# Kernel optimization log

Measured on AMD Instinct MI355X. Metric: run time of the kernel, lower is better.

## Reference

```python
import jax, jax.numpy as jnp
import numpy as np

B, S, D = 16, 512, 2048
NUM_HEADS, NUM_GROUPS = 16, 4
HEAD_DIM = D // NUM_HEADS  # 128
MAX_SEQ_LEN, SHARED_SLOTS = 512, 32
EPS = 1e-6


def _rope_tables(seq_positions):
    # inv_freq over half the head dim, as in the module
    inv_freq = 1.0 / (10000.0 ** (jnp.arange(0, HEAD_DIM, 2, dtype=jnp.float32) / HEAD_DIM))
    freqs = jnp.outer(seq_positions.astype(jnp.float32), inv_freq)  # [S, HEAD_DIM//2]
    return jnp.cos(freqs), jnp.sin(freqs)


def _apply_rope(x, cos, sin):
    # x: [b, s, h, head_dim]; cos/sin: [s, 1, head_dim//2] (broadcast over heads)
    x1, x2 = jnp.split(x, 2, axis=-1)
    real = x1 * cos - x2 * sin
    imag = x1 * sin + x2 * cos
    return jnp.concatenate([real, imag], axis=-1).astype(x.dtype)


def _rmsnorm(x, scale):
    # flax RMSNorm with dtype=float32: compute in fp32
    x = x.astype(jnp.float32)
    ms = jnp.mean(jnp.square(x), axis=-1, keepdims=True)
    return x * jax.lax.rsqrt(ms + EPS) * scale


def setup_inputs() -> dict:
    key = jax.random.key(0)
    ks = jax.random.split(key, 10)
    w = 0.02
    return {
        "x": jax.random.normal(ks[0], (B, S, D), dtype=jnp.float32),
        "wq": jax.random.normal(ks[1], (D, D), dtype=jnp.float32) * w,
        "bq": jnp.zeros((D,), dtype=jnp.float32),
        "wk": jax.random.normal(ks[2], (D, NUM_GROUPS * HEAD_DIM), dtype=jnp.float32) * w,
        "bk": jnp.zeros((NUM_GROUPS * HEAD_DIM,), dtype=jnp.float32),
        "wv": jax.random.normal(ks[3], (D, NUM_GROUPS * HEAD_DIM), dtype=jnp.float32) * w,
        "bv": jnp.zeros((NUM_GROUPS * HEAD_DIM,), dtype=jnp.float32),
        "wo": jax.random.normal(ks[4], (D, D), dtype=jnp.float32) * w,
        "bo": jnp.zeros((D,), dtype=jnp.float32),
        "q_norm_scale": jnp.ones((HEAD_DIM,), dtype=jnp.float32),
        "k_norm_scale": jnp.ones((HEAD_DIM,), dtype=jnp.float32),
    }


def reference(x, wq, bq, wk, bk, wv, bv, wo, bo, q_norm_scale, k_norm_scale):
    b, s, d = x.shape
    rep = NUM_HEADS // NUM_GROUPS
    head_scale = HEAD_DIM ** (-0.5)  # applied once explicitly by the module

    # nnx.Linear(dtype=float16): projections computed in fp16
    xh = x.astype(jnp.float16)
    q = (xh @ wq.astype(jnp.float16) + bq.astype(jnp.float16)).reshape(b, s, NUM_HEADS, HEAD_DIM)
    k = (xh @ wk.astype(jnp.float16) + bk.astype(jnp.float16)).reshape(b, s, NUM_GROUPS, HEAD_DIM)
    v = (xh @ wv.astype(jnp.float16) + bv.astype(jnp.float16)).reshape(b, s, NUM_GROUPS, HEAD_DIM)

    # QK RMSNorm (fp32)
    q = _rmsnorm(q, q_norm_scale)
    k = _rmsnorm(k, k_norm_scale)

    # RoPE (default positions 0..s-1)
    pos = jnp.arange(s)
    cos, sin = _rope_tables(pos)
    cos = cos[:, None, :]
    sin = sin[:, None, :]
    q = _apply_rope(q, cos, sin) * head_scale
    k = _apply_rope(k, cos, sin)

    q = q.astype(jnp.float16)
    k = k.astype(jnp.float16)
    v = v.astype(jnp.float16)

    # GQA without materializing repeated k/v: [b, s, groups, rep, head_dim]
    qg = q.reshape(b, s, NUM_GROUPS, rep, HEAD_DIM)
    # dot_product_attention applies its own 1/sqrt(head_dim) (double-scale, faithful)
    logits = jnp.einsum('btgrh,bsgh->bgrts', qg, k,
                        preferred_element_type=jnp.float32) * head_scale

    causal = pos[:, None] >= pos[None, :]  # [s, s]
    logits = jnp.where(causal[None, None, None, :, :], logits, jnp.finfo(jnp.float32).min)
    probs = jax.nn.softmax(logits, axis=-1).astype(jnp.float16)

    out = jnp.einsum('bgrts,bsgh->btgrh', probs, v)  # [b, s, groups, rep, head_dim]
    out = out.reshape(b, s, d)
    return out @ wo.astype(jnp.float16) + bo.astype(jnp.float16)
```

## Files before the change

kernel.cpp:

```cpp
#include <hip/hip_runtime.h>

#define NB 16
#define NS 512
#define ND 2048
#define NH 16
#define NG 4
#define NHD 128
#define NM (NB * NS)
#define NKD (NG * NHD)
#define NKV 1024
#define HEAD_SCALE 0.08838834764831845f

typedef _Float16 h8 __attribute__((ext_vector_type(8)));
typedef float fx4 __attribute__((ext_vector_type(4)));

__device__ __forceinline__ void gload16(const void* g, void* l) {
  __builtin_amdgcn_global_load_lds(
      (__attribute__((address_space(1))) void*)(unsigned long long)g,
      (__attribute__((address_space(3))) void*)(unsigned long long)l,
      16, 0, 0);
}


__global__ void prep_kernel(const float* __restrict__ x, _Float16* __restrict__ xh,
                            const float* __restrict__ wq, _Float16* __restrict__ wqt,
                            const float* __restrict__ wk, const float* __restrict__ wv,
                            _Float16* __restrict__ wkvt,
                            const float* __restrict__ wo, _Float16* __restrict__ wot,
                            float* __restrict__ cosT, float* __restrict__ sinT,
                            const float* __restrict__ bk, const float* __restrict__ bv,
                            float* __restrict__ bkv) {
  __shared__ float t[64][65];
  const int bid = blockIdx.x, tid = threadIdx.x;
  if (bid < 2048) {
    const fx4* p = (const fx4*)x;
    h8* o = (h8*)xh;
#pragma unroll
    for (int it = 0; it < 4; ++it) {
      int i = (it * 2048 + bid) * 256 + tid;
      fx4 a = p[2 * i], b = p[2 * i + 1];
      h8 hv;
      hv[0] = (_Float16)a[0]; hv[1] = (_Float16)a[1]; hv[2] = (_Float16)a[2]; hv[3] = (_Float16)a[3];
      hv[4] = (_Float16)b[0]; hv[5] = (_Float16)b[1]; hv[6] = (_Float16)b[2]; hv[7] = (_Float16)b[3];
      o[i] = hv;
    }
    return;
  }
  int lb = bid - 2048;
  const float* src;
  _Float16* dst;
  int K, N;
  if (lb < 1024)      { src = wq; dst = wqt; K = ND; N = ND; }
  else if (lb < 1280) { lb -= 1024; src = wk; dst = wkvt; K = ND; N = NKD; }
  else if (lb < 1536) { lb -= 1280; src = wv; dst = wkvt + (size_t)NKD * ND; K = ND; N = NKD; }
  else if (lb < 2560) { lb -= 1536; src = wo; dst = wot; K = ND; N = ND; }
  else if (lb < 2688) {
    int i = (lb - 2560) * 256 + tid;
    int s = i >> 6, f = i & 63;
    float inv = exp2f(-(float)f * (13.287712379549449f / 64.0f));
    float a = (float)s * inv;
    cosT[i] = cosf(a);
    sinT[i] = sinf(a);
    return;
  } else {
#pragma unroll
    for (int it = 0; it < 4; ++it) {
      int idx = it * 256 + tid;
      bkv[idx] = (idx < NKD) ? bk[idx] : bv[idx - NKD];
    }
    return;
  }
  const int ntil = N >> 6;
  const int n0 = (lb % ntil) * 64, k0 = (lb / ntil) * 64;
#pragma unroll
  for (int it = 0; it < 16; ++it) {
    int idx = it * 256 + tid;
    int r = idx >> 6, c = idx & 63;
    t[r][c] = src[(size_t)(k0 + r) * N + n0 + c];
  }
  __syncthreads();
#pragma unroll
  for (int it = 0; it < 16; ++it) {
    int idx = it * 256 + tid;
    int r = idx >> 6, c = idx & 63;
    dst[(size_t)(n0 + r) * K + k0 + c] = (_Float16)t[c][r];
  }
}


__global__ void kv_post_kernel(_Float16* __restrict__ kv, _Float16* __restrict__ vt,
                               const float* __restrict__ kns,
                               const float* __restrict__ cosT, const float* __restrict__ sinT) {
  __shared__ _Float16 t[64][72];
  const int bid = blockIdx.x, tid = threadIdx.x;
  if (bid < 8192) {
    int wid = tid >> 6, lane = tid & 63;
    int task = bid * 4 + wid;
    int row = task >> 2;
    int head = task & 3;
    _Float16* p = kv + (size_t)row * NKV + head * NHD;
    float x1 = (float)p[lane], x2 = (float)p[lane + 64];
    float ss = x1 * x1 + x2 * x2;
#pragma unroll
    for (int m = 1; m < 64; m <<= 1) ss += __shfl_xor(ss, m, 64);
    float rn = rsqrtf(ss * (1.0f / 128.0f) + 1e-6f);
    int s = row & (NS - 1);
    float c = cosT[s * 64 + lane], sn = sinT[s * 64 + lane];
    float n1 = x1 * rn * kns[lane], n2 = x2 * rn * kns[64 + lane];
    p[lane] = (_Float16)(n1 * c - n2 * sn);
    p[lane + 64] = (_Float16)(n1 * sn + n2 * c);
    return;
  }
  const int v = bid - 8192;
  const int st = v & 7, dt = (v >> 3) & 1, bg = v >> 4;
  const int b = bg >> 2, g = bg & 3;
  const _Float16* src = kv + ((size_t)(b * NS + st * 64)) * NKV + NKD + g * NHD + dt * 64;
#pragma unroll
  for (int it = 0; it < 2; ++it) {
    int idx = it * 256 + tid;
    int r = idx >> 3, c = (idx & 7) * 8;
    *(h8*)&t[r][c] = *(const h8*)(src + (size_t)r * NKV + c);
  }
  __syncthreads();
  _Float16* dst = vt + ((size_t)bg * NHD + dt * 64) * NS + st * 64;
#pragma unroll
  for (int it = 0; it < 2; ++it) {
    int idx = it * 256 + tid;
    int r = idx >> 3, c = (idx & 7) * 8;
    h8 o;
#pragma unroll
    for (int e = 0; e < 8; ++e) o[e] = t[c + e][r];
    *(h8*)(dst + (size_t)r * NS + c) = o;
  }
}

__device__ __forceinline__ void st_out(float* p, float v) { *p = v; }
__device__ __forceinline__ void st_out(_Float16* p, float v) { *p = (_Float16)v; }


template <typename OT>
__global__ __launch_bounds__(256, 3) void gemm_bt_kernel(
    const _Float16* __restrict__ A, const _Float16* __restrict__ Bt,
    const float* __restrict__ bias, OT* __restrict__ C, int N, int K) {
  __shared__ alignas(16) _Float16 As[128 * 64];
  __shared__ alignas(16) _Float16 Bs[128 * 64];
  const int tid = threadIdx.x;
  const int lane = tid & 63, wid = tid >> 6;
  const int wr = wid >> 1, wc = wid & 1;
  const int la = lane & 15, lb = (lane >> 4) * 8;
  const int bm = blockIdx.y * 128, bn = blockIdx.x * 128;

  fx4 acc[4][4] = {};

  for (int kt = 0; kt < K; kt += 64) {
    const _Float16* Ag = A + (size_t)bm * K + kt;
    const _Float16* Bg = Bt + (size_t)bn * K + kt;
#pragma unroll
    for (int it = 0; it < 4; ++it) {
      int cb = it * 256 + wid * 64;
      int ca = cb + lane;
      int r = ca >> 3, cc = ca & 7;
      gload16(Ag + (size_t)r * K + cc * 8, &As[cb * 8]);
      gload16(Bg + (size_t)r * K + cc * 8, &Bs[cb * 8]);
    }
    __syncthreads();
#pragma unroll
    for (int kk = 0; kk < 2; ++kk) {
      h8 af[4], bf[4];
#pragma unroll
      for (int m = 0; m < 4; ++m)
        af[m] = *(const h8*)&As[(wr * 64 + m * 16 + la) * 64 + kk * 32 + lb];
#pragma unroll
      for (int n = 0; n < 4; ++n)
        bf[n] = *(const h8*)&Bs[(wc * 64 + n * 16 + la) * 64 + kk * 32 + lb];
#pragma unroll
      for (int m = 0; m < 4; ++m)
#pragma unroll
        for (int n = 0; n < 4; ++n)
          acc[m][n] = __builtin_amdgcn_mfma_f32_16x16x32_f16(af[m], bf[n], acc[m][n], 0, 0, 0);
    }
    __syncthreads();
  }
#pragma unroll
  for (int m = 0; m < 4; ++m) {
    int row0 = bm + wr * 64 + m * 16 + (lane >> 4) * 4;
#pragma unroll
    for (int n = 0; n < 4; ++n) {
      int col = bn + wc * 64 + n * 16 + la;
      float bvv = bias[col];
#pragma unroll
      for (int r = 0; r < 4; ++r)
        st_out(&C[(size_t)(row0 + r) * N + col], acc[m][n][r] + bvv);
    }
  }
}


template <typename OT>
__global__ __launch_bounds__(512, 2) void gemm256_kernel(
    const _Float16* __restrict__ A, const _Float16* __restrict__ Bt,
    const float* __restrict__ bias, OT* __restrict__ C, int N, int K) {
  __shared__ alignas(16) _Float16 As[2][2][256 * 32];
  __shared__ alignas(16) _Float16 Bs[2][2][256 * 32];
  const int tid = threadIdx.x;
  const int lane = tid & 63, w = tid >> 6;
  const int wr = w >> 2, wc = w & 3;
  const int la = lane & 15, lq = lane >> 4;
  const int lin = (blockIdx.x & 7) * 32 + (blockIdx.x >> 3);
  const int nbx = N >> 8;
  const int by = lin / nbx, bx = lin % nbx;
  const int bm = by * 256, bn = bx * 256;
  const int NT = K >> 6;

  fx4 acc[8][4] = {};

  {
    const _Float16* Ag = A + (size_t)bm * K;
    const _Float16* Bg = Bt + (size_t)bn * K;
#pragma unroll
    for (int sh = 0; sh < 2; ++sh) {
#pragma unroll
      for (int i = 0; i < 2; ++i) {
        int cb = i * 512 + w * 64;
        int s = cb + lane;
        int r = s >> 2, c = s & 3;
        gload16(Ag + (size_t)r * K + sh * 32 + ((c ^ ((r >> 1) & 3)) << 3), &As[0][sh][cb * 8]);
      }
#pragma unroll
      for (int i = 0; i < 2; ++i) {
        int cb = i * 512 + w * 64;
        int s = cb + lane;
        int r = s >> 2, c = s & 3;
        gload16(Bg + (size_t)r * K + sh * 32 + ((c ^ ((r >> 1) & 3)) << 3), &Bs[0][sh][cb * 8]);
      }
    }
  }
  asm volatile("s_waitcnt vmcnt(4)" ::: "memory");
  __builtin_amdgcn_s_barrier();

  for (int kt = 0; kt < NT; ++kt) {
    const int cur = kt & 1;
    const int nxt = cur ^ 1;
    const bool more = (kt + 1 < NT);
    const _Float16* Ag = A + (size_t)bm * K + (kt + 1) * 64;
    const _Float16* Bg = Bt + (size_t)bn * K + (kt + 1) * 64;
    h8 bf[4];
#pragma unroll
    for (int ph = 0; ph < 4; ++ph) {
      const int kh = ph >> 1, g = ph & 1;
      h8 af[4];
#pragma unroll
      for (int mi = 0; mi < 4; ++mi) {
        int row = wr * 128 + (g * 4 + mi) * 16 + la;
        af[mi] = *(const h8*)&As[cur][kh][row * 32 + ((lq ^ ((row >> 1) & 3)) << 3)];
      }
      if (g == 0) {
#pragma unroll
        for (int ni = 0; ni < 4; ++ni) {
          int row = wc * 64 + ni * 16 + la;
          bf[ni] = *(const h8*)&Bs[cur][kh][row * 32 + ((lq ^ ((row >> 1) & 3)) << 3)];
        }
      }
      if (more) {
        const int sh = ph >> 1;
        const _Float16* Sg = (ph & 1) ? Bg : Ag;
        _Float16* Ld = (ph & 1) ? &Bs[nxt][sh][0] : &As[nxt][sh][0];
#pragma unroll
        for (int i = 0; i < 2; ++i) {
          int cb = i * 512 + w * 64;
          int s = cb + lane;
          int r = s >> 2, c = s & 3;
          gload16(Sg + (size_t)r * K + sh * 32 + ((c ^ ((r >> 1) & 3)) << 3), Ld + cb * 8);
        }
      }
      if (ph == 1 || ph == 3) {
        if (more) asm volatile("s_waitcnt vmcnt(4)" ::: "memory");
        else      asm volatile("s_waitcnt vmcnt(0)" ::: "memory");
      }
      __builtin_amdgcn_s_barrier();
      asm volatile("s_waitcnt lgkmcnt(0)" ::: "memory");
      __builtin_amdgcn_sched_barrier(0);
      __builtin_amdgcn_s_setprio(1);
#pragma unroll
      for (int mi = 0; mi < 4; ++mi)
#pragma unroll
        for (int ni = 0; ni < 4; ++ni)
          acc[g * 4 + mi][ni] = __builtin_amdgcn_mfma_f32_16x16x32_f16(
              af[mi], bf[ni], acc[g * 4 + mi][ni], 0, 0, 0);
      __builtin_amdgcn_s_setprio(0);
      __builtin_amdgcn_sched_barrier(0);
      __builtin_amdgcn_s_barrier();
    }
  }
#pragma unroll
  for (int mi = 0; mi < 8; ++mi) {
    int row0 = bm + wr * 128 + mi * 16 + lq * 4;
#pragma unroll
    for (int ni = 0; ni < 4; ++ni) {
      int col = bn + wc * 64 + ni * 16 + la;
      float bvv = bias[col];
#pragma unroll
      for (int r = 0; r < 4; ++r)
        st_out(&C[(size_t)(row0 + r) * N + col], acc[mi][ni][r] + bvv);
    }
  }
}


__global__ __launch_bounds__(512, 4) void attn_kernel(
    const _Float16* __restrict__ Q, const _Float16* __restrict__ KV,
    const _Float16* __restrict__ Vt, _Float16* __restrict__ ctx,
    const float* __restrict__ qns, const float* __restrict__ cosT,
    const float* __restrict__ sinT) {
  __shared__ alignas(16) _Float16 Ks[2][64 * 128];
  __shared__ alignas(16) _Float16 Vs[2][128 * 64];
  __shared__ alignas(16) _Float16 Ps[8][16 * 64];

  const int bid = blockIdx.x;
  const int logical = (bid & 7) * 64 + (bid >> 3);
  const int b = logical >> 5;
  const int g = (logical >> 3) & 3;
  const int jp = logical & 7;
  const int j1 = jp, j2 = 15 - jp;

  const int tid = threadIdx.x;
  const int lane = tid & 63, w = tid >> 6;
  const int la = lane & 15, lq = lane >> 4;
  const int h = g * 4 + (w & 3);
  const int rh = w >> 2;

  const _Float16* Vg = Vt + (size_t)(b * NG + g) * NHD * NS;

  auto stage = [&](int buf, int kt) {
    const _Float16* Kg = KV + ((size_t)(b * NS + kt * 64)) * NKV + g * NHD;
#pragma unroll
    for (int it = 0; it < 2; ++it) {
      int cb = it * 512 + w * 64;
      int s = cb + lane;
      int rr = s >> 4, c = s & 15;
      gload16(Kg + (size_t)rr * NKV + ((c ^ (rr & 7)) * 8), &Ks[buf][cb * 8]);
    }
#pragma unroll
    for (int it = 0; it < 2; ++it) {
      int cb = it * 512 + w * 64;
      int s = cb + lane;
      int rr = s >> 3, c = s & 7;
      gload16(Vg + (size_t)rr * NS + kt * 64 + ((c ^ (rr & 7)) * 8), &Vs[buf][cb * 8]);
    }
  };

  const int nt1 = ((j1 * 32 + 31) >> 6) + 1;
  const int nt2 = ((j2 * 32 + 31) >> 6) + 1;
  const int ntotal = nt1 + nt2;

  h8 qf[4];
  fx4 oacc[8];
  float mrun[4], lrun[4];

  stage(0, 0);
  int cur = 0;
  for (int t = 0; t < ntotal; ++t) {
    const bool inA = t < nt1;
    const int j = inA ? j1 : j2;
    const int kt = inA ? t : t - nt1;
    const int ntj = inA ? nt1 : nt2;
    __syncthreads();
    if (t + 1 < ntotal) {
      int nkt = (t + 1 < nt1) ? (t + 1) : (t + 1 - nt1);
      stage(cur ^ 1, nkt);
    }
    if (kt == 0) {
      const int qrow = j * 32 + rh * 16 + la;
      const _Float16* Qg = Q + ((size_t)(b * NS + qrow)) * ND + h * NHD + lq * 8;
      float xq[4][8];
      float ss = 0.f;
#pragma unroll
      for (int kc = 0; kc < 4; ++kc) {
        h8 v = *(const h8*)(Qg + kc * 32);
#pragma unroll
        for (int e = 0; e < 8; ++e) { xq[kc][e] = (float)v[e]; ss += xq[kc][e] * xq[kc][e]; }
      }
      ss += __shfl_xor(ss, 16, 64);
      ss += __shfl_xor(ss, 32, 64);
      float rn = rsqrtf(ss * (1.0f / 128.0f) + 1e-6f);
#pragma unroll
      for (int kc = 0; kc < 2; ++kc) {
        const float* s1p = qns + kc * 32 + lq * 8;
        const float* s2p = qns + (kc + 2) * 32 + lq * 8;
        const float* ctp = cosT + qrow * 64 + kc * 32 + lq * 8;
        const float* stp = sinT + qrow * 64 + kc * 32 + lq * 8;
        fx4 s1a = *(const fx4*)s1p, s1b = *(const fx4*)(s1p + 4);
        fx4 s2a = *(const fx4*)s2p, s2b = *(const fx4*)(s2p + 4);
        fx4 ca = *(const fx4*)ctp, cb2 = *(const fx4*)(ctp + 4);
        fx4 sa = *(const fx4*)stp, sb = *(const fx4*)(stp + 4);
#pragma unroll
        for (int e = 0; e < 8; ++e) {
          float sc1 = (e < 4) ? s1a[e & 3] : s1b[e & 3];
          float sc2 = (e < 4) ? s2a[e & 3] : s2b[e & 3];
          float cc = (e < 4) ? ca[e & 3] : cb2[e & 3];
          float sn = (e < 4) ? sa[e & 3] : sb[e & 3];
          float n1 = xq[kc][e] * rn * sc1;
          float n2 = xq[kc + 2][e] * rn * sc2;
          qf[kc][e] = (_Float16)((n1 * cc - n2 * sn) * HEAD_SCALE);
          qf[kc + 2][e] = (_Float16)((n1 * sn + n2 * cc) * HEAD_SCALE);
        }
      }
#pragma unroll
      for (int f = 0; f < 8; ++f) oacc[f] = fx4{0.f, 0.f, 0.f, 0.f};
#pragma unroll
      for (int r = 0; r < 4; ++r) { mrun[r] = -1e30f; lrun[r] = 0.f; }
    }

    fx4 sc[4] = {};
    __builtin_amdgcn_s_setprio(1);
#pragma unroll
    for (int n = 0; n < 4; ++n) {
      int row = n * 16 + la;
#pragma unroll
      for (int kc = 0; kc < 4; ++kc) {
        h8 bk = *(const h8*)&Ks[cur][row * 128 + (((kc * 4 + lq) ^ (la & 7)) * 8)];
        sc[n] = __builtin_amdgcn_mfma_f32_16x16x32_f16(qf[kc], bk, sc[n], 0, 0, 0);
      }
    }
    __builtin_amdgcn_s_setprio(0);

    const int qrow0 = j * 32 + rh * 16 + lq * 4;
    const bool maskT = (kt == ntj - 1);
    float pv[4][4];
    float rm[4] = {-1e30f, -1e30f, -1e30f, -1e30f};
#pragma unroll
    for (int n = 0; n < 4; ++n) {
      int kv = kt * 64 + n * 16 + la;
#pragma unroll
      for (int r = 0; r < 4; ++r) {
        float sv = sc[n][r] * HEAD_SCALE;
        sv = (maskT && kv > qrow0 + r) ? -1e30f : sv;
        pv[n][r] = sv;
        rm[r] = fmaxf(rm[r], sv);
      }
    }
#pragma unroll
    for (int r = 0; r < 4; ++r)
#pragma unroll
      for (int m = 1; m < 16; m <<= 1) rm[r] = fmaxf(rm[r], __shfl_xor(rm[r], m, 64));
    bool defer = (rm[0] - mrun[0] <= 8.f) && (rm[1] - mrun[1] <= 8.f) &&
                 (rm[2] - mrun[2] <= 8.f) && (rm[3] - mrun[3] <= 8.f);
    if (!__all(defer)) {
#pragma unroll
      for (int r = 0; r < 4; ++r) {
        float mn = fmaxf(mrun[r], rm[r]);
        float corr = __expf(mrun[r] - mn);
        mrun[r] = mn;
        lrun[r] *= corr;
#pragma unroll
        for (int f = 0; f < 8; ++f) oacc[f][r] *= corr;
      }
    }
    float rs[4] = {0.f, 0.f, 0.f, 0.f};
#pragma unroll
    for (int n = 0; n < 4; ++n)
#pragma unroll
      for (int r = 0; r < 4; ++r) {
        float e = __expf(pv[n][r] - mrun[r]);
        pv[n][r] = e;
        rs[r] += e;
      }
#pragma unroll
    for (int r = 0; r < 4; ++r) {
#pragma unroll
      for (int m = 1; m < 16; m <<= 1) rs[r] += __shfl_xor(rs[r], m, 64);
      lrun[r] += rs[r];
    }

#pragma unroll
    for (int n = 0; n < 4; ++n)
#pragma unroll
      for (int r = 0; r < 4; ++r) {
        int row = lq * 4 + r;
        int chsw = (n * 2 + (la >> 3)) ^ (row & 7);
        Ps[w][row * 64 + chsw * 8 + (la & 7)] = (_Float16)pv[n][r];
      }
    asm volatile("s_waitcnt lgkmcnt(0)" ::: "memory");
    __builtin_amdgcn_sched_barrier(0);
    h8 pf[2];
#pragma unroll
    for (int ks = 0; ks < 2; ++ks)
      pf[ks] = *(const h8*)&Ps[w][la * 64 + (((ks * 4 + lq) ^ (la & 7)) * 8)];

    __builtin_amdgcn_s_setprio(1);
#pragma unroll
    for (int f = 0; f < 8; ++f) {
      int row = f * 16 + la;
#pragma unroll
      for (int ks = 0; ks < 2; ++ks) {
        h8 bv = *(const h8*)&Vs[cur][row * 64 + (((ks * 4 + lq) ^ (la & 7)) * 8)];
        oacc[f] = __builtin_amdgcn_mfma_f32_16x16x32_f16(pf[ks], bv, oacc[f], 0, 0, 0);
      }
    }
    __builtin_amdgcn_s_setprio(0);

    if (maskT) {
      _Float16* Cg = ctx + ((size_t)(b * NS + qrow0)) * ND + h * NHD + la;
      float inv_l[4];
#pragma unroll
      for (int r = 0; r < 4; ++r) inv_l[r] = 1.0f / lrun[r];
#pragma unroll
      for (int f = 0; f < 8; ++f)
#pragma unroll
        for (int r = 0; r < 4; ++r)
          Cg[(size_t)r * ND + f * 16] = (_Float16)(oacc[f][r] * inv_l[r]);
    }
    cur ^= 1;
  }
}


extern "C" void kernel_launch(void* const* d_in, const int* in_sizes, int n_in,
                              void* d_out, int out_size, void* d_ws, size_t ws_size,
                              hipStream_t stream) {
  (void)in_sizes; (void)n_in; (void)out_size; (void)ws_size;
  const float* x = (const float*)d_in[0];
  const float* wq = (const float*)d_in[1];
  const float* bq = (const float*)d_in[2];
  const float* wk = (const float*)d_in[3];
  const float* bk = (const float*)d_in[4];
  const float* wv = (const float*)d_in[5];
  const float* bv = (const float*)d_in[6];
  const float* wo = (const float*)d_in[7];
  const float* bo = (const float*)d_in[8];
  const float* qns = (const float*)d_in[9];
  const float* kns = (const float*)d_in[10];

  char* ws = (char*)d_ws;
  size_t off = 0;
  _Float16* xh = (_Float16*)(ws + off); off += (size_t)NM * ND * 2;
  _Float16* wqt = (_Float16*)(ws + off); off += (size_t)ND * ND * 2;
  _Float16* wkvt = (_Float16*)(ws + off); off += (size_t)NKV * ND * 2;
  _Float16* wot = (_Float16*)(ws + off); off += (size_t)ND * ND * 2;
  _Float16* Qb = (_Float16*)(ws + off); off += (size_t)NM * ND * 2;
  _Float16* KVbuf = (_Float16*)(ws + off); off += (size_t)NM * NKV * 2;
  float* cosT = (float*)(ws + off); off += (size_t)NS * 64 * 4;
  float* sinT = (float*)(ws + off); off += (size_t)NS * 64 * 4;
  float* bkv = (float*)(ws + off); off += (size_t)NKV * 4;
  _Float16* ctx = xh;
  _Float16* Vtg = wqt;

  prep_kernel<<<dim3(4737), 256, 0, stream>>>(x, xh, wq, wqt, wk, wv, wkvt, wo, wot,
                                              cosT, sinT, bk, bv, bkv);

  gemm256_kernel<_Float16><<<dim3(256), dim3(512), 0, stream>>>(xh, wqt, bq, Qb, ND, ND);
  gemm_bt_kernel<_Float16><<<dim3(NKV / 128, NM / 128), 256, 0, stream>>>(xh, wkvt, bkv, KVbuf, NKV, ND);

  kv_post_kernel<<<dim3(9216), 256, 0, stream>>>(KVbuf, Vtg, kns, cosT, sinT);

  attn_kernel<<<dim3(512), dim3(512), 0, stream>>>(Qb, KVbuf, Vtg, ctx, qns, cosT, sinT);

  gemm256_kernel<float><<<dim3(256), dim3(512), 0, stream>>>(ctx, wot, bo, (float*)d_out, ND, ND);
}
```

Before: 301.3 us.

## Use pipelined 256x128 GEMM for KV projection and skip fully masked attention subtiles

Replaces the simple single-buffered 128x128 KV-projection GEMM with a 256x128-tile, double-buffered, swizzled-LDS pipelined kernel modeled on the Q-projection GEMM. This is meant to cut global-load stalls and barrier overhead for the KV projection. The attention kernel also skips the QK MFMAs, masking and exp work for 16-column key subtiles that lie entirely above the causal diagonal in the last tile, zeroing their probabilities. The changes add code complexity and rely on the grid mapping of 256 blocks matching the problem sizes.

```diff
diff --git a/kernel.cpp b/kernel.cpp
--- a/kernel.cpp
+++ b/kernel.cpp
@@ -139,64 +139,6 @@
 
 
 template <typename OT>
-__global__ __launch_bounds__(256, 3) void gemm_bt_kernel(
-    const _Float16* __restrict__ A, const _Float16* __restrict__ Bt,
-    const float* __restrict__ bias, OT* __restrict__ C, int N, int K) {
-  __shared__ alignas(16) _Float16 As[128 * 64];
-  __shared__ alignas(16) _Float16 Bs[128 * 64];
-  const int tid = threadIdx.x;
-  const int lane = tid & 63, wid = tid >> 6;
-  const int wr = wid >> 1, wc = wid & 1;
-  const int la = lane & 15, lb = (lane >> 4) * 8;
-  const int bm = blockIdx.y * 128, bn = blockIdx.x * 128;
-
-  fx4 acc[4][4] = {};
-
-  for (int kt = 0; kt < K; kt += 64) {
-    const _Float16* Ag = A + (size_t)bm * K + kt;
-    const _Float16* Bg = Bt + (size_t)bn * K + kt;
-#pragma unroll
-    for (int it = 0; it < 4; ++it) {
-      int cb = it * 256 + wid * 64;
-      int ca = cb + lane;
-      int r = ca >> 3, cc = ca & 7;
-      gload16(Ag + (size_t)r * K + cc * 8, &As[cb * 8]);
-      gload16(Bg + (size_t)r * K + cc * 8, &Bs[cb * 8]);
-    }
-    __syncthreads();
-#pragma unroll
-    for (int kk = 0; kk < 2; ++kk) {
-      h8 af[4], bf[4];
-#pragma unroll
-      for (int m = 0; m < 4; ++m)
-        af[m] = *(const h8*)&As[(wr * 64 + m * 16 + la) * 64 + kk * 32 + lb];
-#pragma unroll
-      for (int n = 0; n < 4; ++n)
-        bf[n] = *(const h8*)&Bs[(wc * 64 + n * 16 + la) * 64 + kk * 32 + lb];
-#pragma unroll
-      for (int m = 0; m < 4; ++m)
-#pragma unroll
-        for (int n = 0; n < 4; ++n)
-          acc[m][n] = __builtin_amdgcn_mfma_f32_16x16x32_f16(af[m], bf[n], acc[m][n], 0, 0, 0);
-    }
-    __syncthreads();
-  }
-#pragma unroll
-  for (int m = 0; m < 4; ++m) {
-    int row0 = bm + wr * 64 + m * 16 + (lane >> 4) * 4;
-#pragma unroll
-    for (int n = 0; n < 4; ++n) {
-      int col = bn + wc * 64 + n * 16 + la;
-      float bvv = bias[col];
-#pragma unroll
-      for (int r = 0; r < 4; ++r)
-        st_out(&C[(size_t)(row0 + r) * N + col], acc[m][n][r] + bvv);
-    }
-  }
-}
-
-
-template <typename OT>
 __global__ __launch_bounds__(512, 2) void gemm256_kernel(
     const _Float16* __restrict__ A, const _Float16* __restrict__ Bt,
     const float* __restrict__ bias, OT* __restrict__ C, int N, int K) {
@@ -307,6 +249,108 @@
 }
 
 
+__global__ __launch_bounds__(512, 2) void gemm256n128_kernel(
+    const _Float16* __restrict__ A, const _Float16* __restrict__ Bt,
+    const float* __restrict__ bias, _Float16* __restrict__ C, int N, int K) {
+  __shared__ alignas(16) _Float16 As[2][2][256 * 32];
+  __shared__ alignas(16) _Float16 Bs[2][2][128 * 32];
+  const int tid = threadIdx.x;
+  const int lane = tid & 63, w = tid >> 6;
+  const int wr = w >> 2, wc = w & 3;
+  const int la = lane & 15, lq = lane >> 4;
+  const int lin = (blockIdx.x & 7) * 32 + (blockIdx.x >> 3);
+  const int nbx = N >> 7;
+  const int by = lin / nbx, bx = lin % nbx;
+  const int bm = by * 256, bn = bx * 128;
+  const int NT = K >> 6;
+
+  fx4 acc[8][2] = {};
+
+  auto stageA = [&](int buf, int kt, int sh) {
+    const _Float16* Ag = A + (size_t)bm * K + kt * 64;
+#pragma unroll
+    for (int i = 0; i < 2; ++i) {
+      int cb = i * 512 + w * 64;
+      int s = cb + lane;
+      int r = s >> 2, c = s & 3;
+      gload16(Ag + (size_t)r * K + sh * 32 + ((c ^ ((r >> 1) & 3)) << 3), &As[buf][sh][cb * 8]);
+    }
+  };
+  auto stageB = [&](int buf, int kt, int sh) {
+    const _Float16* Bg = Bt + (size_t)bn * K + kt * 64;
+    int s = w * 64 + lane;
+    int r = s >> 2, c = s & 3;
+    gload16(Bg + (size_t)r * K + sh * 32 + ((c ^ ((r >> 1) & 3)) << 3),
+            &Bs[buf][sh][(w * 64) * 8]);
+  };
+
+  stageA(0, 0, 0);
+  stageB(0, 0, 0);
+  stageA(0, 0, 1);
+  stageB(0, 0, 1);
+  asm volatile("s_waitcnt vmcnt(3)" ::: "memory");
+  __builtin_amdgcn_s_barrier();
+
+  for (int kt = 0; kt < NT; ++kt) {
+    const int cur = kt & 1;
+    const int nxt = cur ^ 1;
+    const bool more = (kt + 1 < NT);
+    h8 bf[2];
+#pragma unroll
+    for (int ph = 0; ph < 4; ++ph) {
+      const int kh = ph >> 1, g = ph & 1;
+      h8 af[4];
+#pragma unroll
+      for (int mi = 0; mi < 4; ++mi) {
+        int row = wr * 128 + (g * 4 + mi) * 16 + la;
+        af[mi] = *(const h8*)&As[cur][kh][row * 32 + ((lq ^ ((row >> 1) & 3)) << 3)];
+      }
+      if (g == 0) {
+#pragma unroll
+        for (int ni = 0; ni < 2; ++ni) {
+          int row = wc * 32 + ni * 16 + la;
+          bf[ni] = *(const h8*)&Bs[cur][kh][row * 32 + ((lq ^ ((row >> 1) & 3)) << 3)];
+        }
+      }
+      if (more) {
+        const int sh = ph >> 1;
+        if (ph & 1) stageB(nxt, kt + 1, sh);
+        else        stageA(nxt, kt + 1, sh);
+      }
+      if (ph == 1 || ph == 3) {
+        if (more) asm volatile("s_waitcnt vmcnt(3)" ::: "memory");
+        else      asm volatile("s_waitcnt vmcnt(0)" ::: "memory");
+      }
+      __builtin_amdgcn_s_barrier();
+      asm volatile("s_waitcnt lgkmcnt(0)" ::: "memory");
+      __builtin_amdgcn_sched_barrier(0);
+      __builtin_amdgcn_s_setprio(1);
+#pragma unroll
+      for (int mi = 0; mi < 4; ++mi)
+#pragma unroll
+        for (int ni = 0; ni < 2; ++ni)
+          acc[g * 4 + mi][ni] = __builtin_amdgcn_mfma_f32_16x16x32_f16(
+              af[mi], bf[ni], acc[g * 4 + mi][ni], 0, 0, 0);
+      __builtin_amdgcn_s_setprio(0);
+      __builtin_amdgcn_sched_barrier(0);
+      __builtin_amdgcn_s_barrier();
+    }
+  }
+#pragma unroll
+  for (int mi = 0; mi < 8; ++mi) {
+    int row0 = bm + wr * 128 + mi * 16 + lq * 4;
+#pragma unroll
+    for (int ni = 0; ni < 2; ++ni) {
+      int col = bn + wc * 32 + ni * 16 + la;
+      float bvv = bias[col];
+#pragma unroll
+      for (int r = 0; r < 4; ++r)
+        C[(size_t)(row0 + r) * N + col] = (_Float16)(acc[mi][ni][r] + bvv);
+    }
+  }
+}
+
+
 __global__ __launch_bounds__(512, 4) void attn_kernel(
     const _Float16* __restrict__ Q, const _Float16* __restrict__ KV,
     const _Float16* __restrict__ Vt, _Float16* __restrict__ ctx,
@@ -411,32 +455,38 @@
       for (int r = 0; r < 4; ++r) { mrun[r] = -1e30f; lrun[r] = 0.f; }
     }
 
+    const bool maskT = (kt == ntj - 1);
+    const int nlim = maskT ? ((((j * 32 + 31) & 63) >> 4) + 1) : 4;
+
     fx4 sc[4] = {};
     __builtin_amdgcn_s_setprio(1);
 #pragma unroll
     for (int n = 0; n < 4; ++n) {
-      int row = n * 16 + la;
-#pragma unroll
-      for (int kc = 0; kc < 4; ++kc) {
-        h8 bk = *(const h8*)&Ks[cur][row * 128 + (((kc * 4 + lq) ^ (la & 7)) * 8)];
-        sc[n] = __builtin_amdgcn_mfma_f32_16x16x32_f16(qf[kc], bk, sc[n], 0, 0, 0);
+      if (n < nlim) {
+        int row = n * 16 + la;
+#pragma unroll
+        for (int kc = 0; kc < 4; ++kc) {
+          h8 bk = *(const h8*)&Ks[cur][row * 128 + (((kc * 4 + lq) ^ (la & 7)) * 8)];
+          sc[n] = __builtin_amdgcn_mfma_f32_16x16x32_f16(qf[kc], bk, sc[n], 0, 0, 0);
+        }
       }
     }
     __builtin_amdgcn_s_setprio(0);
 
     const int qrow0 = j * 32 + rh * 16 + lq * 4;
-    const bool maskT = (kt == ntj - 1);
     float pv[4][4];
     float rm[4] = {-1e30f, -1e30f, -1e30f, -1e30f};
 #pragma unroll
     for (int n = 0; n < 4; ++n) {
-      int kv = kt * 64 + n * 16 + la;
-#pragma unroll
-      for (int r = 0; r < 4; ++r) {
-        float sv = sc[n][r] * HEAD_SCALE;
-        sv = (maskT && kv > qrow0 + r) ? -1e30f : sv;
-        pv[n][r] = sv;
-        rm[r] = fmaxf(rm[r], sv);
+      if (n < nlim) {
+        int kv = kt * 64 + n * 16 + la;
+#pragma unroll
+        for (int r = 0; r < 4; ++r) {
+          float sv = sc[n][r] * HEAD_SCALE;
+          sv = (maskT && kv > qrow0 + r) ? -1e30f : sv;
+          pv[n][r] = sv;
+          rm[r] = fmaxf(rm[r], sv);
+        }
       }
     }
 #pragma unroll
@@ -458,13 +508,19 @@
     }
     float rs[4] = {0.f, 0.f, 0.f, 0.f};
 #pragma unroll
-    for (int n = 0; n < 4; ++n)
-#pragma unroll
-      for (int r = 0; r < 4; ++r) {
-        float e = __expf(pv[n][r] - mrun[r]);
-        pv[n][r] = e;
-        rs[r] += e;
-      }
+    for (int n = 0; n < 4; ++n) {
+      if (n < nlim) {
+#pragma unroll
+        for (int r = 0; r < 4; ++r) {
+          float e = __expf(pv[n][r] - mrun[r]);
+          pv[n][r] = e;
+          rs[r] += e;
+        }
+      } else {
+#pragma unroll
+        for (int r = 0; r < 4; ++r) pv[n][r] = 0.f;
+      }
+    }
 #pragma unroll
     for (int r = 0; r < 4; ++r) {
 #pragma unroll
@@ -549,7 +605,7 @@
                                               cosT, sinT, bk, bv, bkv);
 
   gemm256_kernel<_Float16><<<dim3(256), dim3(512), 0, stream>>>(xh, wqt, bq, Qb, ND, ND);
-  gemm_bt_kernel<_Float16><<<dim3(NKV / 128, NM / 128), 256, 0, stream>>>(xh, wkvt, bkv, KVbuf, NKV, ND);
+  gemm256n128_kernel<<<dim3(256), dim3(512), 0, stream>>>(xh, wkvt, bkv, KVbuf, NKV, ND);
 
   kv_post_kernel<<<dim3(9216), 256, 0, stream>>>(KVbuf, Vtg, kns, cosT, sinT);
 
```

Result: slower. 312.2 us (+3.6%).
